# Kernel optimization log

Measured on AMD Instinct MI355X. Metric: run time of the kernel, lower is better.

The kernel has to match this reference:

```python
import jax, jax.numpy as jnp
import numpy as np

GROUPS = 32
EPS = 1e-6


def group_norm(x, gamma, beta):
    b, c, h, w = x.shape
    xg = x.reshape(b, GROUPS, c // GROUPS, h, w)
    mu = xg.mean(axis=(2, 3, 4), keepdims=True)
    var = xg.var(axis=(2, 3, 4), keepdims=True)
    xn = ((xg - mu) * jax.lax.rsqrt(var + EPS)).reshape(b, c, h, w)
    return xn * gamma[None, :, None, None] + beta[None, :, None, None]


def conv1x1(x, w, b):
    # x: (b,c_in,h,w), w: (c_out,c_in), b: (c_out,)
    return jnp.einsum('oc,bchw->bohw', w, x) + b[None, :, None, None]


def setup_inputs() -> dict:
    key = jax.random.key(0)
    ks = jax.random.split(key, 10)
    c = 512
    scale = 1.0 / np.sqrt(c)
    inp = jax.random.normal(ks[0], (16, c, 32, 32), dtype=jnp.float32)
    return {
        'inp': inp,
        'gamma': jnp.ones((c,), jnp.float32),
        'beta': jnp.zeros((c,), jnp.float32),
        'Wq': jax.random.normal(ks[1], (c, c), jnp.float32) * scale,
        'bq': jnp.zeros((c,), jnp.float32),
        'Wk': jax.random.normal(ks[2], (c, c), jnp.float32) * scale,
        'bk': jnp.zeros((c,), jnp.float32),
        'Wv': jax.random.normal(ks[3], (c, c), jnp.float32) * scale,
        'bv': jnp.zeros((c,), jnp.float32),
        'Wo': jax.random.normal(ks[4], (c, c), jnp.float32) * scale,
        'bo': jnp.zeros((c,), jnp.float32),
    }


def reference(inp, gamma, beta, Wq, bq, Wk, bk, Wv, bv, Wo, bo):
    b, c, h, w = inp.shape
    x = group_norm(inp, gamma, beta)
    Q = conv1x1(x, Wq, bq).reshape(b, c, h * w)  # (b,c,n)
    K = conv1x1(x, Wk, bk).reshape(b, c, h * w)  # (b,c,m)
    V = conv1x1(x, Wv, bv).reshape(b, c, h * w)  # (b,c,m)
    # attn[b,n,m] = sum_c Q[b,c,n] * K[b,c,m], scaled then softmax over m
    attn = jnp.einsum('bcn,bcm->bnm', Q, K) / jnp.sqrt(jnp.float32(c))
    attn = jax.nn.softmax(attn, axis=2)
    # A[b,c,n] = sum_m V[b,c,m] * attn[b,n,m]  (== bmm(V, attn^T))
    A = jnp.einsum('bcm,bnm->bcn', V, attn).reshape(b, c, h, w)
    A = conv1x1(A, Wo, bo)
    return inp + A
```

## Files before the change

kernel.cpp:

```cpp
#include <hip/hip_runtime.h>

typedef unsigned short UST;
typedef __attribute__((ext_vector_type(8))) short bf16x8;
typedef __attribute__((ext_vector_type(8))) unsigned short us8;
typedef __attribute__((ext_vector_type(4))) float f32x4;

__device__ __forceinline__ UST f2bf(float f) {
  union { float f; unsigned int u; } x; x.f = f;
  unsigned int r = x.u + 0x7fffu + ((x.u >> 16) & 1u);
  return (UST)(r >> 16);
}
__device__ __forceinline__ float bf2f(UST h) {
  union { unsigned int u; float f; } x; x.u = ((unsigned int)h) << 16;
  return x.f;
}

__device__ __forceinline__ void sync_lds() {
  asm volatile("s_waitcnt lgkmcnt(0)\n\ts_barrier" ::: "memory");
}
__device__ __forceinline__ void barrier_nowait() {
  asm volatile("s_barrier" ::: "memory");
}

typedef const __attribute__((address_space(1))) void g_void;
typedef __attribute__((address_space(3))) void lds_void;
__device__ __forceinline__ void gload16(const UST* g, UST* l) {
  __builtin_amdgcn_global_load_lds((g_void*)g, (lds_void*)l, 16, 0, 0);
}

__global__ __launch_bounds__(256) void prep(
    const float* __restrict__ inp, const float* __restrict__ gamma,
    const float* __restrict__ beta, UST* __restrict__ Xnt,
    const float4* __restrict__ wq, const float4* __restrict__ wk,
    const float4* __restrict__ wv, const float4* __restrict__ wo,
    ushort4* __restrict__ oqkv, ushort4* __restrict__ owo,
    const float4* __restrict__ bq4, const float4* __restrict__ bk4,
    const float4* __restrict__ bv4, float4* __restrict__ bqkv4,
    float4* __restrict__ l4) {
  const int tid = threadIdx.x;
  if (blockIdx.x >= 768) {
    int i = (blockIdx.x - 768) * 256 + tid;
    l4[i] = make_float4(0.f, 0.f, 0.f, 0.f);
    return;
  }
  if (blockIdx.x >= 512) {
    const int wb = blockIdx.x - 512;
    int i = wb * 256 + tid;
    float4 v;
    v = wq[i]; oqkv[i]          = make_ushort4(f2bf(v.x), f2bf(v.y), f2bf(v.z), f2bf(v.w));
    v = wk[i]; oqkv[i + 65536]  = make_ushort4(f2bf(v.x), f2bf(v.y), f2bf(v.z), f2bf(v.w));
    v = wv[i]; oqkv[i + 131072] = make_ushort4(f2bf(v.x), f2bf(v.y), f2bf(v.z), f2bf(v.w));
    v = wo[i]; owo[i]           = make_ushort4(f2bf(v.x), f2bf(v.y), f2bf(v.z), f2bf(v.w));
    if (wb < 2) {
      int t = wb * 256 + tid;
      if (t < 384) bqkv4[t] = (t < 128) ? bq4[t] : (t < 256 ? bk4[t - 128] : bv4[t - 256]);
    }
    return;
  }
  const int g = blockIdx.x & 31, b = blockIdx.x >> 5;
  const float4* p4 = (const float4*)(inp + ((size_t)b * 32 + g) * 16384);
  float x[16][4];
  float s = 0.f, ss = 0.f;
#pragma unroll
  for (int i = 0; i < 16; i++) {
    float4 t = p4[tid + i * 256];
    x[i][0] = t.x; x[i][1] = t.y; x[i][2] = t.z; x[i][3] = t.w;
    s += t.x + t.y + t.z + t.w;
    ss += t.x * t.x + t.y * t.y + t.z * t.z + t.w * t.w;
  }
  for (int o = 32; o >= 1; o >>= 1) { s += __shfl_xor(s, o); ss += __shfl_xor(ss, o); }
  __shared__ float red[8];
  __shared__ float mu_s, rstd_s;
  const int w = tid >> 6;
  if ((tid & 63) == 0) { red[w * 2] = s; red[w * 2 + 1] = ss; }
  __syncthreads();
  if (tid == 0) {
    float S1 = red[0] + red[2] + red[4] + red[6];
    float S2 = red[1] + red[3] + red[5] + red[7];
    float mu = S1 * (1.f / 16384.f);
    float var = S2 * (1.f / 16384.f) - mu * mu;
    mu_s = mu; rstd_s = rsqrtf(var + 1e-6f);
  }
  __syncthreads();
  const float mu = mu_s, rstd = rstd_s;
#pragma unroll
  for (int o2 = 0; o2 < 2; o2++) {
    const int ccg = g * 2 + o2;
    float sc[8], sh[8];
#pragma unroll
    for (int j = 0; j < 8; j++) {
      int ch = ccg * 8 + j;
      sc[j] = gamma[ch] * rstd;
      sh[j] = beta[ch] - mu * sc[j];
    }
#pragma unroll
    for (int m = 0; m < 4; m++) {
      us8 v;
#pragma unroll
      for (int j = 0; j < 8; j++) v[j] = f2bf(x[o2 * 8 + j][m] * sc[j] + sh[j]);
      *(us8*)(Xnt + (size_t)b * 524288 + (size_t)ccg * 8192 + (size_t)(4 * tid + m) * 8) = v;
    }
  }
}

template <int EPI, int NT, int AR>
__global__ __launch_bounds__(512, 2) void gemm8p(
    const UST* __restrict__ A, const UST* __restrict__ B, void* __restrict__ C,
    const float* __restrict__ bias, const float* __restrict__ extra, float scale,
    int K, int ldc, int rsA, int csA, long ssA, int rsB, long ssB,
    long zA, long zB, long zC) {
  __shared__ __align__(16) UST buf[65536];

  const int tid = threadIdx.x;
  int lin = blockIdx.x + NT * (blockIdx.y + gridDim.y * blockIdx.z);
  int T = gridDim.y * gridDim.z;
  int per = T >> 3;
  int g = lin & 7, idx = lin >> 3;
  int at = g * per + idx / NT;
  int x = idx % NT;
  const int m0 = (at % gridDim.y) * 256;
  const int z = at / gridDim.y;
  const int n0 = x * 256;

  const UST* Ab = A + (long)z * zA;
  const UST* Bb = B + (long)z * zB;

  const int w = tid >> 6, lane = tid & 63;
  const int quad = lane >> 4, l16 = lane & 15;
  const int wr = w >> 2, wc = w & 3;

  f32x4 acc[8][4];
#pragma unroll
  for (int i = 0; i < 8; i++)
#pragma unroll
    for (int j = 0; j < 4; j++) acc[i][j] = f32x4{0.f, 0.f, 0.f, 0.f};

  const UST* gp[8];
  int lo[8];
  {
    const int lr = w * 8 + (lane >> 3);
    const int kcl = (lane & 7) ^ (lane >> 3);
#pragma unroll
    for (int p = 0; p < 8; p++) {
      int q;
      bool isA;
      if (p == 0) { q = 0; isA = true; }
      else if (p == 1) { q = 2; isA = true; }
      else if (p == 6) { q = 1; isA = true; }
      else if (p == 7) { q = 3; isA = true; }
      else { q = p - 2; isA = false; }
      if (isA) {
        if (AR) gp[p] = Ab + (size_t)(m0 + q * 64 + lane) * rsA + (size_t)w * csA;
        else    gp[p] = Ab + (size_t)(m0 + q * 64 + lr) * rsA + (size_t)kcl * csA;
        lo[p] = q * 4096 + w * 512;
      } else {
        gp[p] = Bb + (size_t)(n0 + q * 64 + lr) * rsB + (size_t)kcl * 8;
        lo[p] = 16384 + q * 4096 + w * 512;
      }
    }
  }

  int aoffs[8][2], boffs[4][2];
#pragma unroll
  for (int i = 0; i < 8; i++) {
    int R = wr * 128 + i * 16 + l16;
    int q = R >> 6, lr = R & 63;
#pragma unroll
    for (int ks = 0; ks < 2; ks++) {
      int kc = ks * 4 + quad;
      aoffs[i][ks] = AR ? (q * 4096 + (kc * 64 + lr) * 8)
                        : (q * 4096 + (lr * 8 + (kc ^ (lr & 7))) * 8);
    }
  }
#pragma unroll
  for (int j = 0; j < 4; j++) {
    int R = wc * 64 + j * 16 + l16;
    int q = R >> 6, lr = R & 63;
#pragma unroll
    for (int ks = 0; ks < 2; ks++) {
      int kc = ks * 4 + quad;
      boffs[j][ks] = 16384 + q * 4096 + (lr * 8 + (kc ^ (lr & 7))) * 8;
    }
  }

  const int nk = K >> 6;

#define STG(P, SS) { gload16(gp[P], lb + lo[P]); gp[P] += (SS); }

  {
    UST* lb = buf;
    STG(0, ssA) STG(1, ssA) STG(2, ssB) STG(3, ssB)
    STG(4, ssB) STG(5, ssB) STG(6, ssA) STG(7, ssA)
  }
  asm volatile("s_waitcnt vmcnt(2)" ::: "memory");
  barrier_nowait();

#define PH(IH, JH, P0, P1, SS0, SS1, VME)                                     \
  {                                                                           \
    bf16x8 af[4][2], bfr[2][2];                                               \
    _Pragma("unroll") for (int il = 0; il < 4; il++)                          \
      _Pragma("unroll") for (int ks = 0; ks < 2; ks++)                        \
        af[il][ks] = *(const bf16x8*)(cb + aoffs[(IH)*4 + il][ks]);           \
    _Pragma("unroll") for (int jl = 0; jl < 2; jl++)                          \
      _Pragma("unroll") for (int ks = 0; ks < 2; ks++)                        \
        bfr[jl][ks] = *(const bf16x8*)(cb + boffs[(JH)*2 + jl][ks]);          \
    if (stg) { STG(P0, SS0) STG(P1, SS1) }                                    \
    barrier_nowait();                                                         \
    asm volatile("s_waitcnt lgkmcnt(0)" ::: "memory");                        \
    __builtin_amdgcn_sched_barrier(0);                                        \
    __builtin_amdgcn_s_setprio(1);                                            \
    _Pragma("unroll") for (int il = 0; il < 4; il++)                          \
      _Pragma("unroll") for (int jl = 0; jl < 2; jl++)                        \
        _Pragma("unroll") for (int ks = 0; ks < 2; ks++)                      \
          acc[(IH)*4 + il][(JH)*2 + jl] = __builtin_amdgcn_mfma_f32_16x16x32_bf16( \
              af[il][ks], bfr[jl][ks], acc[(IH)*4 + il][(JH)*2 + jl], 0, 0, 0);    \
    __builtin_amdgcn_s_setprio(0);                                            \
    VME;                                                                      \
    barrier_nowait();                                                         \
  }

  for (int t = 0; t < nk; ++t) {
    const UST* cb = buf + (t & 1) * 32768;
    UST* lb = buf + ((t + 1) & 1) * 32768;
    const bool stg = (t + 1 < nk);
    PH(0, 0, 0, 1, ssA, ssA, {})
    PH(0, 1, 2, 3, ssB, ssB, {
      if (stg) { asm volatile("s_waitcnt vmcnt(4)" ::: "memory"); }
      else     { asm volatile("s_waitcnt vmcnt(0)" ::: "memory"); }
    })
    PH(1, 0, 4, 5, ssB, ssB, {})
    PH(1, 1, 6, 7, ssA, ssA, {
      if (stg) { asm volatile("s_waitcnt vmcnt(2)" ::: "memory"); }
    })
  }
#undef PH
#undef STG

  if constexpr (EPI == 7) {
    UST* Cb = (UST*)C + (long)z * zC;
    float* lrow = (float*)extra + (long)z * 1024;
#pragma unroll
    for (int h = 0; h < 2; ++h) {
      if (h) barrier_nowait();
      if (wr == h) {
#pragma unroll
        for (int i = 0; i < 8; i++)
#pragma unroll
          for (int j = 0; j < 4; j++)
#pragma unroll
            for (int r = 0; r < 4; r++) {
              float v = __expf(acc[i][j][r] * scale);
              buf[(i * 16 + quad * 4 + r) * 260 + wc * 64 + j * 16 + l16] = f2bf(v);
            }
      }
      sync_lds();
#pragma unroll
      for (int it = 0; it < 8; ++it) {
        int q = tid + it * 512;
        int row = q >> 5, colc = q & 31;
        us8 v = *(us8*)&buf[row * 260 + colc * 8];
        *(us8*)&Cb[(size_t)(m0 + h * 128 + row) * ldc + n0 + colc * 8] = v;
        float s = 0.f;
#pragma unroll
        for (int jj = 0; jj < 8; jj++) s += bf2f(v[jj]);
        s += __shfl_xor(s, 16); s += __shfl_xor(s, 8);
        s += __shfl_xor(s, 4); s += __shfl_xor(s, 2); s += __shfl_xor(s, 1);
        if ((lane & 31) == 0) atomicAdd(&lrow[m0 + h * 128 + row], s);
      }
    }
  } else {
    const bool vreg = (n0 >= 1024);
    if (!vreg) {
      UST* Cb = (UST*)C + (long)z * zC;
#pragma unroll
      for (int h = 0; h < 2; ++h) {
        if (h) barrier_nowait();
        if (wr == h) {
#pragma unroll
          for (int i = 0; i < 8; i++)
#pragma unroll
            for (int j = 0; j < 4; j++) {
              const float bc = bias[n0 + wc * 64 + j * 16 + l16];
#pragma unroll
              for (int r = 0; r < 4; r++)
                buf[(i * 16 + quad * 4 + r) * 260 + wc * 64 + j * 16 + l16] =
                    f2bf(acc[i][j][r] + bc);
            }
        }
        sync_lds();
#pragma unroll
        for (int it = 0; it < 8; ++it) {
          int q = tid + it * 512;
          int row = q >> 5, colc = q & 31;
          us8 v = *(us8*)&buf[row * 260 + colc * 8];
          *(us8*)&Cb[(size_t)(m0 + h * 128 + row) * ldc + n0 + colc * 8] = v;
        }
      }
    } else {
      UST* Vb = (UST*)extra + (long)z * 524288;
#pragma unroll
      for (int h = 0; h < 2; ++h) {
        if (h) barrier_nowait();
        if ((wc >> 1) == h) {
#pragma unroll
          for (int i = 0; i < 8; i++)
#pragma unroll
            for (int j = 0; j < 4; j++) {
              const float bc = bias[n0 + wc * 64 + j * 16 + l16];
              const int Cl = (wc & 1) * 64 + j * 16 + l16;
              const int R0 = wr * 128 + i * 16 + quad * 4;
              ushort4 sv;
              sv.x = f2bf(acc[i][j][0] + bc);
              sv.y = f2bf(acc[i][j][1] + bc);
              sv.z = f2bf(acc[i][j][2] + bc);
              sv.w = f2bf(acc[i][j][3] + bc);
              *(ushort4*)&buf[Cl * 260 + R0] = sv;
            }
        }
        sync_lds();
#pragma unroll
        for (int it = 0; it < 8; ++it) {
          int q = tid + it * 512;
          int Cl = q >> 5, mc = q & 31;
          us8 v = *(us8*)&buf[Cl * 260 + mc * 8];
          *(us8*)&Vb[(size_t)(n0 - 1024 + h * 128 + Cl) * 1024 + m0 + mc * 8] = v;
        }
      }
    }
  }
}

template <int EPI, int NT, int AR, int BR>
__global__ __launch_bounds__(256, 4) void gemm_bt(
    const UST* __restrict__ A, const UST* __restrict__ B, void* __restrict__ C,
    const float* __restrict__ bias, const float* __restrict__ extra, float scale,
    int K, int ldc,
    int rsA, int csA, int ssA, int rsB, int csB, int ssB,
    long zA, long zB, long zC) {
  __shared__ __align__(16) UST buf[16384];

  const int tid = threadIdx.x;
  int m0, n0, z;
  if constexpr (NT > 0) {
    int lin = blockIdx.x + NT * (blockIdx.y + gridDim.y * blockIdx.z);
    int T = gridDim.y * gridDim.z;
    int per = T >> 3;
    int g = lin & 7, idx = lin >> 3;
    int at = g * per + idx / NT;
    int x = idx % NT;
    m0 = (at % gridDim.y) * 128; z = at / gridDim.y; n0 = x * 128;
  } else {
    m0 = blockIdx.y * 128; n0 = blockIdx.x * 128; z = blockIdx.z;
  }
  const UST* Ab = A + (long)z * zA;
  const UST* Bb = B + (long)z * zB;

  const int w = tid >> 6, lane = tid & 63;
  const int quad = lane >> 4, l16 = lane & 15;
  const int wm = w >> 1, wn = w & 1;

  f32x4 acc[4][4];
#pragma unroll
  for (int i = 0; i < 4; i++)
#pragma unroll
    for (int j = 0; j < 4; j++) acc[i][j] = f32x4{0.f, 0.f, 0.f, 0.f};

  const UST* gA[2];
  const UST* gB[2];
#pragma unroll
  for (int t = 0; t < 2; t++) {
    int q = t * 256 + w * 64 + lane;
    int row, kc;
    if constexpr (AR) { kc = q >> 7; row = q & 127; }
    else {
      row = q >> 2; int kk = q & 3;
      kc = kk ^ (((row >> 1) ^ (row >> 3)) & 3);
    }
    gA[t] = Ab + (size_t)(m0 + row) * rsA + (size_t)kc * csA;
  }
#pragma unroll
  for (int t = 0; t < 2; t++) {
    int q = t * 256 + w * 64 + lane;
    int row, kc;
    if constexpr (BR) { kc = q >> 7; row = q & 127; }
    else {
      row = q >> 2; int kk = q & 3;
      kc = kk ^ (((row >> 1) ^ (row >> 3)) & 3);
    }
    gB[t] = Bb + (size_t)(n0 + row) * rsB + (size_t)kc * csB;
  }
  int aoff[4], boff[4];
#pragma unroll
  for (int i = 0; i < 4; i++) {
    int R = wm * 64 + i * 16 + l16;
    if constexpr (AR) aoff[i] = quad * 1024 + R * 8;
    else {
      int s = ((R >> 1) ^ (R >> 3)) & 3;
      aoff[i] = R * 32 + (quad ^ s) * 8;
    }
  }
#pragma unroll
  for (int j = 0; j < 4; j++) {
    int R = wn * 64 + j * 16 + l16;
    if constexpr (BR) boff[j] = quad * 1024 + R * 8;
    else {
      int s = ((R >> 1) ^ (R >> 3)) & 3;
      boff[j] = R * 32 + (quad ^ s) * 8;
    }
  }

  const int nk = K >> 5;

#define STAGE(bb)                                   \
  {                                                 \
    UST* sA = buf + (bb) * 8192;                    \
    UST* sB = sA + 4096;                            \
    _Pragma("unroll") for (int t = 0; t < 2; t++) { \
      gload16(gA[t], sA + t * 2048 + w * 512);      \
      gA[t] += ssA;                                 \
    }                                               \
    _Pragma("unroll") for (int t = 0; t < 2; t++) { \
      gload16(gB[t], sB + t * 2048 + w * 512);      \
      gB[t] += ssB;                                 \
    }                                               \
  }

  STAGE(0)
  STAGE(1)

  for (int k = 0; k < nk; ++k) {
    if (k + 1 < nk) asm volatile("s_waitcnt vmcnt(4)" ::: "memory");
    else            asm volatile("s_waitcnt vmcnt(0)" ::: "memory");
    barrier_nowait();
    const UST* cA = buf + (k & 1) * 8192;
    const UST* cB = cA + 4096;
    bf16x8 af[4], bfr[4];
#pragma unroll
    for (int i = 0; i < 4; i++) af[i] = *(const bf16x8*)(cA + aoff[i]);
#pragma unroll
    for (int j = 0; j < 4; j++) bfr[j] = *(const bf16x8*)(cB + boff[j]);
    __builtin_amdgcn_s_setprio(1);
#pragma unroll
    for (int i = 0; i < 4; i++)
#pragma unroll
      for (int j = 0; j < 4; j++)
        acc[i][j] = __builtin_amdgcn_mfma_f32_16x16x32_bf16(af[i], bfr[j], acc[i][j], 0, 0, 0);
    __builtin_amdgcn_s_setprio(0);
    if (k + 2 < nk) {
      sync_lds();
      STAGE(k & 1)
    }
  }
  sync_lds();

  if constexpr (EPI == 4) {
    float* fbuf = (float*)buf;
    float* Cb = (float*)C + (long)z * zC;
    const float* Eb = extra + (long)z * zC;
#pragma unroll
    for (int p = 0; p < 4; ++p) {
      if (p) barrier_nowait();
      if (wm == (p >> 1)) {
#pragma unroll
        for (int ii = 0; ii < 2; ii++) {
          const int i = (p & 1) * 2 + ii;
#pragma unroll
          for (int j = 0; j < 4; j++)
#pragma unroll
            for (int r = 0; r < 4; r++)
              fbuf[(ii * 16 + quad * 4 + r) * 132 + wn * 64 + j * 16 + l16] = acc[i][j][r];
        }
      }
      sync_lds();
#pragma unroll
      for (int it = 0; it < 4; ++it) {
        int q = tid + it * 256;
        int row = q >> 5, colc = q & 31;
        int gr = m0 + p * 32 + row;
        size_t off = (size_t)gr * ldc + n0 + colc * 4;
        float4 v = *(float4*)&fbuf[row * 132 + colc * 4];
        float4 e = *(const float4*)&Eb[off];
        float bb = bias[gr];
        v.x += bb + e.x; v.y += bb + e.y; v.z += bb + e.z; v.w += bb + e.w;
        *(float4*)&Cb[off] = v;
      }
    }
  } else if constexpr (EPI == 8) {
    UST* Cb = (UST*)C + (long)z * zC;
    const float* lrow = bias + (long)z * 1024;
#pragma unroll
    for (int h = 0; h < 2; ++h) {
      if (h) barrier_nowait();
      if (wm == h) {
#pragma unroll
        for (int i = 0; i < 4; i++) {
          float rs[4];
#pragma unroll
          for (int r = 0; r < 4; r++)
            rs[r] = 1.0f / lrow[m0 + h * 64 + i * 16 + quad * 4 + r];
#pragma unroll
          for (int j = 0; j < 4; j++)
#pragma unroll
            for (int r = 0; r < 4; r++)
              buf[(i * 16 + quad * 4 + r) * 136 + wn * 64 + j * 16 + l16] =
                  f2bf(acc[i][j][r] * rs[r]);
        }
      }
      sync_lds();
#pragma unroll
      for (int it = 0; it < 4; ++it) {
        int q = tid + it * 256;
        int row = q >> 4, colc = q & 15;
        us8 v = *(us8*)&buf[row * 136 + colc * 8];
        *(us8*)&Cb[(size_t)(m0 + h * 64 + row) * ldc + n0 + colc * 8] = v;
      }
    }
  }
#undef STAGE
}

extern "C" void kernel_launch(void* const* d_in, const int* in_sizes, int n_in,
                              void* d_out, int out_size, void* d_ws, size_t ws_size,
                              hipStream_t stream) {
  const float* inp   = (const float*)d_in[0];
  const float* gamma = (const float*)d_in[1];
  const float* beta  = (const float*)d_in[2];
  const float* Wq    = (const float*)d_in[3];
  const float* bq    = (const float*)d_in[4];
  const float* Wk    = (const float*)d_in[5];
  const float* bk    = (const float*)d_in[6];
  const float* Wv    = (const float*)d_in[7];
  const float* bv    = (const float*)d_in[8];
  const float* Wo    = (const float*)d_in[9];
  const float* bo    = (const float*)d_in[10];
  float* out = (float*)d_out;
  char* ws = (char*)d_ws;

  UST*   Xnt   = (UST*)(ws);
  UST*   QKt   = (UST*)(ws + ((size_t)16 << 20));
  UST*   V     = (UST*)(ws + ((size_t)48 << 20));
  UST*   P     = (UST*)(ws + ((size_t)64 << 20));
  float* bqkv  = (float*)(ws + ((size_t)96 << 20));
  UST*   Wqkvb = (UST*)(ws + ((size_t)96 << 20) + 8192);
  UST*   Wob   = Wqkvb + 786432;
  float* l     = (float*)(ws + ((size_t)100 << 20));
  UST*   At    = Xnt;

  prep<<<784, 256, 0, stream>>>(
      inp, gamma, beta, Xnt,
      (const float4*)Wq, (const float4*)Wk, (const float4*)Wv, (const float4*)Wo,
      (ushort4*)Wqkvb, (ushort4*)Wob,
      (const float4*)bq, (const float4*)bk, (const float4*)bv, (float4*)bqkv,
      (float4*)l);

  gemm8p<6, 6, 1><<<dim3(6, 4, 16), 512, 0, stream>>>(
      Xnt, Wqkvb, QKt, bqkv, (const float*)V, 1.f,
      512, 1024, 8, 8192, 65536, 512, 64, 524288, 0, 1048576);
  gemm8p<7, 4, 0><<<dim3(4, 4, 16), 512, 0, stream>>>(
      QKt, QKt + 512, P, nullptr, (const float*)l, 0.04419417382415922f,
      512, 1024, 1024, 8, 64, 1024, 64, 1048576, 1048576, 1048576);
  gemm_bt<8, 4, 0, 0><<<dim3(4, 8, 16), 256, 0, stream>>>(
      P, V, At, (const float*)l, nullptr, 1.f,
      1024, 512, 1024, 8, 32, 1024, 8, 32, 1048576, 524288, 524288);
  gemm_bt<4, 8, 0, 0><<<dim3(8, 4, 16), 256, 0, stream>>>(
      Wob, At, out, bo, inp, 1.f,
      512, 1024, 512, 8, 32, 512, 8, 32, 0, 524288, 524288);
}
```

Baseline: 241.1 us.

## Move QKV projection to 128x128 gemm_bt tiles and restructure gemm8p main loop

The QKV projection GEMM now runs on the smaller-tile gemm_bt kernel (256 threads, 12x8x16 grid) instead of the 256x256 gemm8p kernel, with the bias and transposed-V epilogues ported into gemm_bt. The gemm8p main loop is restructured from four quarter-phases into two half-phases: all B fragments are loaded once and reused across both A halves, with fewer barriers per k-step. The aim is more blocks for better CU occupancy on the QKV GEMM and less sync overhead in the attention-score GEMM. In exchange, gemm_bt reuses less data per loaded tile, and gemm8p holds more fragment registers live at once.

```diff
diff --git a/kernel.cpp b/kernel.cpp
--- a/kernel.cpp
+++ b/kernel.cpp
@@ -195,45 +195,61 @@
   asm volatile("s_waitcnt vmcnt(2)" ::: "memory");
   barrier_nowait();
 
-#define PH(IH, JH, P0, P1, SS0, SS1, VME)                                     \
-  {                                                                           \
-    bf16x8 af[4][2], bfr[2][2];                                               \
-    _Pragma("unroll") for (int il = 0; il < 4; il++)                          \
-      _Pragma("unroll") for (int ks = 0; ks < 2; ks++)                        \
-        af[il][ks] = *(const bf16x8*)(cb + aoffs[(IH)*4 + il][ks]);           \
-    _Pragma("unroll") for (int jl = 0; jl < 2; jl++)                          \
-      _Pragma("unroll") for (int ks = 0; ks < 2; ks++)                        \
-        bfr[jl][ks] = *(const bf16x8*)(cb + boffs[(JH)*2 + jl][ks]);          \
-    if (stg) { STG(P0, SS0) STG(P1, SS1) }                                    \
-    barrier_nowait();                                                         \
-    asm volatile("s_waitcnt lgkmcnt(0)" ::: "memory");                        \
-    __builtin_amdgcn_sched_barrier(0);                                        \
-    __builtin_amdgcn_s_setprio(1);                                            \
-    _Pragma("unroll") for (int il = 0; il < 4; il++)                          \
-      _Pragma("unroll") for (int jl = 0; jl < 2; jl++)                        \
-        _Pragma("unroll") for (int ks = 0; ks < 2; ks++)                      \
-          acc[(IH)*4 + il][(JH)*2 + jl] = __builtin_amdgcn_mfma_f32_16x16x32_bf16( \
-              af[il][ks], bfr[jl][ks], acc[(IH)*4 + il][(JH)*2 + jl], 0, 0, 0);    \
-    __builtin_amdgcn_s_setprio(0);                                            \
-    VME;                                                                      \
-    barrier_nowait();                                                         \
-  }
-
   for (int t = 0; t < nk; ++t) {
     const UST* cb = buf + (t & 1) * 32768;
     UST* lb = buf + ((t + 1) & 1) * 32768;
     const bool stg = (t + 1 < nk);
-    PH(0, 0, 0, 1, ssA, ssA, {})
-    PH(0, 1, 2, 3, ssB, ssB, {
-      if (stg) { asm volatile("s_waitcnt vmcnt(4)" ::: "memory"); }
-      else     { asm volatile("s_waitcnt vmcnt(0)" ::: "memory"); }
-    })
-    PH(1, 0, 4, 5, ssB, ssB, {})
-    PH(1, 1, 6, 7, ssA, ssA, {
-      if (stg) { asm volatile("s_waitcnt vmcnt(2)" ::: "memory"); }
-    })
-  }
-#undef PH
+
+    bf16x8 a0[4][2], bb[4][2];
+#pragma unroll
+    for (int il = 0; il < 4; il++)
+#pragma unroll
+      for (int ks = 0; ks < 2; ks++)
+        a0[il][ks] = *(const bf16x8*)(cb + aoffs[il][ks]);
+#pragma unroll
+    for (int j = 0; j < 4; j++)
+#pragma unroll
+      for (int ks = 0; ks < 2; ks++)
+        bb[j][ks] = *(const bf16x8*)(cb + boffs[j][ks]);
+    if (stg) { STG(0, ssA) STG(1, ssA) STG(2, ssB) STG(3, ssB) }
+    asm volatile("s_waitcnt lgkmcnt(0)" ::: "memory");
+    __builtin_amdgcn_sched_barrier(0);
+    __builtin_amdgcn_s_setprio(1);
+#pragma unroll
+    for (int ks = 0; ks < 2; ks++)
+#pragma unroll
+      for (int il = 0; il < 4; il++)
+#pragma unroll
+        for (int j = 0; j < 4; j++)
+          acc[il][j] = __builtin_amdgcn_mfma_f32_16x16x32_bf16(
+              a0[il][ks], bb[j][ks], acc[il][j], 0, 0, 0);
+    __builtin_amdgcn_s_setprio(0);
+    if (stg) asm volatile("s_waitcnt vmcnt(4)" ::: "memory");
+    else     asm volatile("s_waitcnt vmcnt(0)" ::: "memory");
+    barrier_nowait();
+
+    bf16x8 a1[4][2];
+#pragma unroll
+    for (int il = 0; il < 4; il++)
+#pragma unroll
+      for (int ks = 0; ks < 2; ks++)
+        a1[il][ks] = *(const bf16x8*)(cb + aoffs[4 + il][ks]);
+    if (stg) { STG(4, ssB) STG(5, ssB) STG(6, ssA) STG(7, ssA) }
+    asm volatile("s_waitcnt lgkmcnt(0)" ::: "memory");
+    __builtin_amdgcn_sched_barrier(0);
+    __builtin_amdgcn_s_setprio(1);
+#pragma unroll
+    for (int ks = 0; ks < 2; ks++)
+#pragma unroll
+      for (int il = 0; il < 4; il++)
+#pragma unroll
+        for (int j = 0; j < 4; j++)
+          acc[4 + il][j] = __builtin_amdgcn_mfma_f32_16x16x32_bf16(
+              a1[il][ks], bb[j][ks], acc[4 + il][j], 0, 0, 0);
+    __builtin_amdgcn_s_setprio(0);
+    if (stg) asm volatile("s_waitcnt vmcnt(2)" ::: "memory");
+    barrier_nowait();
+  }
 #undef STG
 
   if constexpr (EPI == 7) {
@@ -266,65 +282,6 @@
         s += __shfl_xor(s, 16); s += __shfl_xor(s, 8);
         s += __shfl_xor(s, 4); s += __shfl_xor(s, 2); s += __shfl_xor(s, 1);
         if ((lane & 31) == 0) atomicAdd(&lrow[m0 + h * 128 + row], s);
-      }
-    }
-  } else {
-    const bool vreg = (n0 >= 1024);
-    if (!vreg) {
-      UST* Cb = (UST*)C + (long)z * zC;
-#pragma unroll
-      for (int h = 0; h < 2; ++h) {
-        if (h) barrier_nowait();
-        if (wr == h) {
-#pragma unroll
-          for (int i = 0; i < 8; i++)
-#pragma unroll
-            for (int j = 0; j < 4; j++) {
-              const float bc = bias[n0 + wc * 64 + j * 16 + l16];
-#pragma unroll
-              for (int r = 0; r < 4; r++)
-                buf[(i * 16 + quad * 4 + r) * 260 + wc * 64 + j * 16 + l16] =
-                    f2bf(acc[i][j][r] + bc);
-            }
-        }
-        sync_lds();
-#pragma unroll
-        for (int it = 0; it < 8; ++it) {
-          int q = tid + it * 512;
-          int row = q >> 5, colc = q & 31;
-          us8 v = *(us8*)&buf[row * 260 + colc * 8];
-          *(us8*)&Cb[(size_t)(m0 + h * 128 + row) * ldc + n0 + colc * 8] = v;
-        }
-      }
-    } else {
-      UST* Vb = (UST*)extra + (long)z * 524288;
-#pragma unroll
-      for (int h = 0; h < 2; ++h) {
-        if (h) barrier_nowait();
-        if ((wc >> 1) == h) {
-#pragma unroll
-          for (int i = 0; i < 8; i++)
-#pragma unroll
-            for (int j = 0; j < 4; j++) {
-              const float bc = bias[n0 + wc * 64 + j * 16 + l16];
-              const int Cl = (wc & 1) * 64 + j * 16 + l16;
-              const int R0 = wr * 128 + i * 16 + quad * 4;
-              ushort4 sv;
-              sv.x = f2bf(acc[i][j][0] + bc);
-              sv.y = f2bf(acc[i][j][1] + bc);
-              sv.z = f2bf(acc[i][j][2] + bc);
-              sv.w = f2bf(acc[i][j][3] + bc);
-              *(ushort4*)&buf[Cl * 260 + R0] = sv;
-            }
-        }
-        sync_lds();
-#pragma unroll
-        for (int it = 0; it < 8; ++it) {
-          int q = tid + it * 512;
-          int Cl = q >> 5, mc = q & 31;
-          us8 v = *(us8*)&buf[Cl * 260 + mc * 8];
-          *(us8*)&Vb[(size_t)(n0 - 1024 + h * 128 + Cl) * 1024 + m0 + mc * 8] = v;
-        }
       }
     }
   }
@@ -513,6 +470,95 @@
         int row = q >> 4, colc = q & 15;
         us8 v = *(us8*)&buf[row * 136 + colc * 8];
         *(us8*)&Cb[(size_t)(m0 + h * 64 + row) * ldc + n0 + colc * 8] = v;
+      }
+    }
+  } else if constexpr (EPI == 7) {
+    UST* Cb = (UST*)C + (long)z * zC;
+    float* lrow = (float*)extra + (long)z * 1024;
+#pragma unroll
+    for (int h = 0; h < 2; ++h) {
+      if (h) barrier_nowait();
+      if (wm == h) {
+#pragma unroll
+        for (int i = 0; i < 4; i++)
+#pragma unroll
+          for (int j = 0; j < 4; j++)
+#pragma unroll
+            for (int r = 0; r < 4; r++) {
+              float v = __expf(acc[i][j][r] * scale);
+              buf[(i * 16 + quad * 4 + r) * 136 + wn * 64 + j * 16 + l16] = f2bf(v);
+            }
+      }
+      sync_lds();
+#pragma unroll
+      for (int it = 0; it < 4; ++it) {
+        int q = tid + it * 256;
+        int row = q >> 4, colc = q & 15;
+        us8 v = *(us8*)&buf[row * 136 + colc * 8];
+        *(us8*)&Cb[(size_t)(m0 + h * 64 + row) * ldc + n0 + colc * 8] = v;
+        float s = 0.f;
+#pragma unroll
+        for (int j = 0; j < 8; j++) s += bf2f(v[j]);
+        s += __shfl_xor(s, 8); s += __shfl_xor(s, 4);
+        s += __shfl_xor(s, 2); s += __shfl_xor(s, 1);
+        if ((lane & 15) == 0) atomicAdd(&lrow[m0 + h * 64 + row], s);
+      }
+    }
+  } else {
+    const bool vreg = (n0 >= 1024);
+    if (!vreg) {
+      UST* Cb = (UST*)C + (long)z * zC;
+#pragma unroll
+      for (int h = 0; h < 2; ++h) {
+        if (h) barrier_nowait();
+        if (wm == h) {
+#pragma unroll
+          for (int i = 0; i < 4; i++)
+#pragma unroll
+            for (int j = 0; j < 4; j++) {
+              const float bc = bias[n0 + wn * 64 + j * 16 + l16];
+#pragma unroll
+              for (int r = 0; r < 4; r++)
+                buf[(i * 16 + quad * 4 + r) * 136 + wn * 64 + j * 16 + l16] =
+                    f2bf(acc[i][j][r] + bc);
+            }
+        }
+        sync_lds();
+#pragma unroll
+        for (int it = 0; it < 4; ++it) {
+          int q = tid + it * 256;
+          int row = q >> 4, colc = q & 15;
+          us8 v = *(us8*)&buf[row * 136 + colc * 8];
+          *(us8*)&Cb[(size_t)(m0 + h * 64 + row) * ldc + n0 + colc * 8] = v;
+        }
+      }
+    } else {
+      UST* Vb = (UST*)extra + (long)z * 524288;
+#pragma unroll
+      for (int h = 0; h < 2; ++h) {
+        if (h) barrier_nowait();
+        if (wn == h) {
+#pragma unroll
+          for (int i = 0; i < 4; i++)
+#pragma unroll
+            for (int j = 0; j < 4; j++) {
+              const float bc = bias[n0 + wn * 64 + j * 16 + l16];
+              ushort4 sv;
+              sv.x = f2bf(acc[i][j][0] + bc);
+              sv.y = f2bf(acc[i][j][1] + bc);
+              sv.z = f2bf(acc[i][j][2] + bc);
+              sv.w = f2bf(acc[i][j][3] + bc);
+              *(ushort4*)&buf[(j * 16 + l16) * 136 + wm * 64 + i * 16 + quad * 4] = sv;
+            }
+        }
+        sync_lds();
+#pragma unroll
+        for (int it = 0; it < 4; ++it) {
+          int q = tid + it * 256;
+          int c = q >> 4, mc = q & 15;
+          us8 v = *(us8*)&buf[c * 136 + mc * 8];
+          *(us8*)&Vb[(size_t)(n0 - 1024 + h * 64 + c) * 1024 + m0 + mc * 8] = v;
+        }
       }
     }
   }
@@ -553,9 +599,9 @@
       (const float4*)bq, (const float4*)bk, (const float4*)bv, (float4*)bqkv,
       (float4*)l);
 
-  gemm8p<6, 6, 1><<<dim3(6, 4, 16), 512, 0, stream>>>(
+  gemm_bt<6, 12, 1, 0><<<dim3(12, 8, 16), 256, 0, stream>>>(
       Xnt, Wqkvb, QKt, bqkv, (const float*)V, 1.f,
-      512, 1024, 8, 8192, 65536, 512, 64, 524288, 0, 1048576);
+      512, 1024, 8, 8192, 32768, 512, 8, 32, 524288, 0, 1048576);
   gemm8p<7, 4, 0><<<dim3(4, 4, 16), 512, 0, stream>>>(
       QKt, QKt + 512, P, nullptr, (const float*)l, 0.04419417382415922f,
       512, 1024, 1024, 8, 64, 1024, 64, 1048576, 1048576, 1048576);
```

After: 215.0 us. -10.8%, faster.
